# Kernel optimization log

Hardware: AMD Instinct MI355X
Metric: run time of the kernel (lower is better)

## Reference

```python
import jax, jax.numpy as jnp
import numpy as np

N_ATOMS = 50000
N_EDGES = 320000
ATOM_DIM = 32
BOND_DIM = 64


def setup_inputs() -> dict:
    key = jax.random.key(0)
    k1, k2, k3, k4 = jax.random.split(key, 4)
    atom_features = jax.random.normal(k1, (N_ATOMS, ATOM_DIM), dtype=jnp.float32)
    bond_features = jax.random.normal(k2, (N_EDGES, BOND_DIM), dtype=jnp.float32)
    pair_indices = jax.random.randint(k3, (N_EDGES, 2), 0, N_ATOMS, dtype=jnp.int64)
    # Xavier-uniform init for kernel [bond_dim, atom_dim*atom_dim]
    fan_in, fan_out = BOND_DIM, ATOM_DIM * ATOM_DIM
    limit = float(np.sqrt(6.0 / (fan_in + fan_out)))
    kernel = jax.random.uniform(k4, (BOND_DIM, ATOM_DIM * ATOM_DIM), dtype=jnp.float32,
                                minval=-limit, maxval=limit)
    bias = jnp.zeros((ATOM_DIM * ATOM_DIM,), dtype=jnp.float32)
    return {"atom_features": atom_features, "bond_features": bond_features,
            "pair_indices": pair_indices, "kernel": kernel, "bias": bias}


def reference(atom_features, bond_features, pair_indices, kernel, bias):
    d = atom_features.shape[-1]
    # Dense projection: [E, bond_dim] @ [bond_dim, d*d] -> [E, d, d]
    edge_mat = (bond_features @ kernel + bias).reshape(-1, d, d)
    # Gather neighbor features and apply per-edge matrix-vector product
    nbr = atom_features[pair_indices[:, 1]]              # [E, d]
    transformed = jnp.einsum('eij,ej->ei', edge_mat, nbr)  # [E, d]
    # Scatter-add aggregation onto destination atoms
    return jax.ops.segment_sum(transformed, pair_indices[:, 0],
                               num_segments=atom_features.shape[0])
```

## Files before the change

### kernel.cpp

```cpp
#include <hip/hip_runtime.h>
#include <stdint.h>

#define NA 50000
#define NE 320000
#define AD 32
#define BD 64

#define WS_FLAG   0
#define WS_COUNTS 16
#define WS_CURSOR (WS_COUNTS + NA)
#define WS_OFFS   (WS_CURSOR + NA)
#define WS_EIDS   150048
#define WS_NEED_PACKED   ((WS_EIDS + 2 * NE) * 4)
#define WS_NEED_UNPACKED ((WS_EIDS + NE) * 4)

__device__ __forceinline__ void load_pair(const void* p, int e, int mode, int& s, int& d){
  if (mode){ const int* q = (const int*)p; s = q[2*e]; d = q[2*e+1]; }
  else     { const long long* q = (const long long*)p; s = (int)q[2*e]; d = (int)q[2*e+1]; }
}

__global__ void k_detect(const void* pairs, uint32_t* ws){
  const uint32_t* w = (const uint32_t*)pairs;
  uint32_t x = 0;
  for (int i = threadIdx.x; i < 2048; i += 256) x |= w[2*i + 1];
  __shared__ uint32_t sh[256];
  sh[threadIdx.x] = x; __syncthreads();
  for (int s = 128; s > 0; s >>= 1){
    if (threadIdx.x < s) sh[threadIdx.x] |= sh[threadIdx.x + s];
    __syncthreads();
  }
  if (threadIdx.x == 0) ws[WS_FLAG] = (sh[0] != 0u) ? 1u : 0u;
}

__global__ void k_hist(const void* pairs, uint32_t* ws){
  int e = blockIdx.x * 256 + threadIdx.x;
  if (e >= NE) return;
  int mode = (int)ws[WS_FLAG];
  int s, d; load_pair(pairs, e, mode, s, d);
  atomicAdd(&ws[WS_COUNTS + s], 1u);
}

__global__ void k_scan(uint32_t* ws){
  const uint32_t* counts = ws + WS_COUNTS;
  uint32_t* offs = ws + WS_OFFS;
  __shared__ uint32_t wsum[16];
  __shared__ uint32_t carrysh;
  const int tid = threadIdx.x; const int lane = tid & 63; const int wid = tid >> 6;
  if (tid == 0) carrysh = 0u;
  __syncthreads();
  for (int base = 0; base < NA; base += 8192){
    uint32_t v[8]; uint32_t tot = 0u;
    int i0 = base + tid * 8;
    #pragma unroll
    for (int j = 0; j < 8; ++j){ int i = i0 + j; v[j] = (i < NA) ? counts[i] : 0u; tot += v[j]; }
    uint32_t inc = tot;
    #pragma unroll
    for (int m = 1; m < 64; m <<= 1){ uint32_t t = __shfl_up(inc, m); if (lane >= m) inc += t; }
    if (lane == 63) wsum[wid] = inc;
    __syncthreads();
    if (wid == 0){
      uint32_t w = (lane < 16) ? wsum[lane] : 0u;
      #pragma unroll
      for (int m = 1; m < 16; m <<= 1){ uint32_t t = __shfl_up(w, m); if (lane >= m) w += t; }
      if (lane < 16) wsum[lane] = w;
    }
    __syncthreads();
    uint32_t waveoff = (wid == 0) ? 0u : wsum[wid - 1];
    uint32_t run = carrysh + waveoff + (inc - tot);
    #pragma unroll
    for (int j = 0; j < 8; ++j){ int i = i0 + j; if (i < NA) offs[i] = run; run += v[j]; }
    __syncthreads();
    if (tid == 0) carrysh += wsum[15];
    __syncthreads();
  }
  if (tid == 0) offs[NA] = carrysh;
}

template<int PACKED>
__global__ void k_scatter(const void* pairs, uint32_t* ws){
  int e = blockIdx.x * 256 + threadIdx.x;
  if (e >= NE) return;
  int mode = (int)ws[WS_FLAG];
  int s, d; load_pair(pairs, e, mode, s, d);
  uint32_t p = atomicAdd(&ws[WS_CURSOR + s], 1u);
  uint32_t pos = ws[WS_OFFS + s] + p;
  if (PACKED) ((uint2*)(ws + WS_EIDS))[pos] = make_uint2((uint32_t)e, (uint32_t)d);
  else        ws[WS_EIDS + pos] = (uint32_t)e;
}

__launch_bounds__(512, 1)
__global__ void k_main(const float* __restrict__ atoms, const float* __restrict__ bonds,
                       const void* __restrict__ pairs, const float* __restrict__ Kg,
                       const float* __restrict__ bias, float* __restrict__ out,
                       const uint32_t* __restrict__ ws, int packed){
  __shared__ float Ksh[8 * 1024];
  __shared__ float red[8 * 520];

  const int tid  = threadIdx.x;
  const int lane = tid & 63;
  const int wid  = tid >> 6;
  const int kk   = lane & 7;
  const int jq   = lane >> 3;
  const int mode = (int)ws[WS_FLAG];
  const uint32_t* offs = ws + WS_OFFS;

  const int a0 = blockIdx.x * 16 + wid * 2;
  const int a1 = a0 + 1;

  float R0[8][4], R1[8][4], S0[4], S1[4];
  #pragma unroll
  for (int c = 0; c < 8; ++c)
    #pragma unroll
    for (int j = 0; j < 4; ++j){ R0[c][j] = 0.f; R1[c][j] = 0.f; }
  #pragma unroll
  for (int j = 0; j < 4; ++j){ S0[j] = 0.f; S1[j] = 0.f; }

  #pragma unroll
  for (int sel = 0; sel < 2; ++sel){
    const int a = sel ? a1 : a0;
    const uint32_t beg = offs[a];
    const uint32_t n   = offs[a + 1] - beg;
    uint32_t e_nxt = 0, d_nxt = 0;
    if (n){
      if (packed){ uint2 ed = ((const uint2*)(ws + WS_EIDS))[beg]; e_nxt = ed.x; d_nxt = ed.y; }
      else {
        e_nxt = ws[WS_EIDS + beg];
        int s_, d_; load_pair(pairs, (int)e_nxt, mode, s_, d_); d_nxt = (uint32_t)d_;
      }
    }
    for (uint32_t t = 0; t < n; ++t){
      const uint32_t e = e_nxt, d = d_nxt;
      if (t + 1 < n){
        if (packed){ uint2 ed = ((const uint2*)(ws + WS_EIDS))[beg + t + 1]; e_nxt = ed.x; d_nxt = ed.y; }
        else {
          e_nxt = ws[WS_EIDS + beg + t + 1];
          int s_, d_; load_pair(pairs, (int)e_nxt, mode, s_, d_); d_nxt = (uint32_t)d_;
        }
      }
      const float4 av = *(const float4*)&atoms[d * AD + jq * 4];
      const float4 b0 = *(const float4*)&bonds[e * BD + kk * 8];
      const float4 b1 = *(const float4*)&bonds[e * BD + kk * 8 + 4];
      const float b[8] = {b0.x, b0.y, b0.z, b0.w, b1.x, b1.y, b1.z, b1.w};
      if (sel == 0){
        #pragma unroll
        for (int c = 0; c < 8; ++c){
          R0[c][0] += b[c] * av.x; R0[c][1] += b[c] * av.y;
          R0[c][2] += b[c] * av.z; R0[c][3] += b[c] * av.w;
        }
        if (kk == 0){ S0[0] += av.x; S0[1] += av.y; S0[2] += av.z; S0[3] += av.w; }
      } else {
        #pragma unroll
        for (int c = 0; c < 8; ++c){
          R1[c][0] += b[c] * av.x; R1[c][1] += b[c] * av.y;
          R1[c][2] += b[c] * av.z; R1[c][3] += b[c] * av.w;
        }
        if (kk == 0){ S1[0] += av.x; S1[1] += av.y; S1[2] += av.z; S1[3] += av.w; }
      }
    }
  }

  float acc0[32], acc1[32];
  #pragma unroll
  for (int i = 0; i < 32; ++i){ acc0[i] = 0.f; acc1[i] = 0.f; }

  #pragma unroll
  for (int c = 0; c < 8; ++c){
    __syncthreads();
    #pragma unroll
    for (int q = 0; q < 4; ++q){
      const int f4   = tid + q * 512;
      const int word = f4 * 4;
      const int row  = word >> 10;
      const int col  = word & 1023;
      const int sw   = row * 1024 + (col ^ (row << 2));
      *(float4*)&Ksh[sw] = *(const float4*)&Kg[(row * 8 + c) * 1024 + col];
    }
    __syncthreads();
    #pragma unroll
    for (int i = 0; i < 32; ++i){
      const float4 kv = *(const float4*)&Ksh[kk * 1024 + ((i * 32 + jq * 4) ^ (kk << 2))];
      acc0[i] += kv.x * R0[c][0] + kv.y * R0[c][1] + kv.z * R0[c][2] + kv.w * R0[c][3];
      acc1[i] += kv.x * R1[c][0] + kv.y * R1[c][1] + kv.z * R1[c][2] + kv.w * R1[c][3];
    }
  }

  if (kk == 0){
    #pragma unroll
    for (int i = 0; i < 32; ++i){
      const float4 bv = *(const float4*)&bias[i * 32 + jq * 4];
      acc0[i] += bv.x * S0[0] + bv.y * S0[1] + bv.z * S0[2] + bv.w * S0[3];
      acc1[i] += bv.x * S1[0] + bv.y * S1[1] + bv.z * S1[2] + bv.w * S1[3];
    }
  }

  float* myred = &red[wid * 520];
  auto epi = [&](const float (&acc)[32], int a){
    #pragma unroll
    for (int g = 0; g < 4; ++g){
      #pragma unroll
      for (int ii = 0; ii < 8; ++ii) myred[ii * 65 + lane] = acc[g * 8 + ii];
      const int ii = lane & 7, seg = lane >> 3;
      float p = 0.f;
      #pragma unroll
      for (int t2 = 0; t2 < 8; ++t2) p += myred[ii * 65 + seg * 8 + t2];
      p += __shfl_xor(p, 8);
      p += __shfl_xor(p, 16);
      p += __shfl_xor(p, 32);
      if (lane < 8) out[a * 32 + g * 8 + lane] = p;
    }
  };
  epi(acc0, a0);
  epi(acc1, a1);
}

extern "C" void kernel_launch(void* const* d_in, const int* in_sizes, int n_in,
                              void* d_out, int out_size, void* d_ws, size_t ws_size,
                              hipStream_t stream){
  const float* atoms = (const float*)d_in[0];
  const float* bonds = (const float*)d_in[1];
  const void*  pairs = d_in[2];
  const float* Kg    = (const float*)d_in[3];
  const float* bias  = (const float*)d_in[4];
  float* out = (float*)d_out;
  uint32_t* ws = (uint32_t*)d_ws;
  const int packed = (ws_size >= (size_t)WS_NEED_PACKED) ? 1 : 0;

  hipMemsetAsync(ws + WS_COUNTS, 0, sizeof(uint32_t) * 2 * NA, stream);
  k_detect<<<1, 256, 0, stream>>>(pairs, ws);
  k_hist<<<(NE + 255) / 256, 256, 0, stream>>>(pairs, ws);
  k_scan<<<1, 1024, 0, stream>>>(ws);
  if (packed) k_scatter<1><<<(NE + 255) / 256, 256, 0, stream>>>(pairs, ws);
  else        k_scatter<0><<<(NE + 255) / 256, 256, 0, stream>>>(pairs, ws);
  k_main<<<NA / 16, 512, 0, stream>>>(atoms, bonds, pairs, Kg, bias, out, ws, packed);
}
```

Measured before the change: 1.156 ms.

## Halve k_main block size and split output accumulation into two halves

k_main now launches 256-thread blocks covering 8 atoms with launch bounds for 2 blocks per CU, instead of 512-thread blocks covering 16 atoms. The K projection stage is split into two halves of 16 output rows, so each thread keeps 16+16 accumulators instead of 32+32 and the shared K tile shrinks to 16 KB. This lowers register and LDS pressure to allow more resident waves and better latency hiding on the gather loop. In exchange, every block streams the full kernel matrix from global memory twice as often, and the half loop adds extra barriers.

```diff
diff --git a/kernel.cpp b/kernel.cpp
--- a/kernel.cpp
+++ b/kernel.cpp
@@ -11,8 +11,7 @@
 #define WS_CURSOR (WS_COUNTS + NA)
 #define WS_OFFS   (WS_CURSOR + NA)
 #define WS_EIDS   150048
-#define WS_NEED_PACKED   ((WS_EIDS + 2 * NE) * 4)
-#define WS_NEED_UNPACKED ((WS_EIDS + NE) * 4)
+#define WS_NEED_PACKED   ((size_t)(WS_EIDS + 2 * NE) * 4)
 
 __device__ __forceinline__ void load_pair(const void* p, int e, int mode, int& s, int& d){
   if (mode){ const int* q = (const int*)p; s = q[2*e]; d = q[2*e+1]; }
@@ -88,13 +87,26 @@
   else        ws[WS_EIDS + pos] = (uint32_t)e;
 }
 
-__launch_bounds__(512, 1)
+#define RUP(Rm, c, bc) { Rm[c][0] += (bc)*av.x; Rm[c][1] += (bc)*av.y; \
+                         Rm[c][2] += (bc)*av.z; Rm[c][3] += (bc)*av.w; }
+
+#define EPI8(accArr, g, a)                                                      \
+  { _Pragma("unroll")                                                           \
+    for (int ii = 0; ii < 8; ++ii) myred[ii * 65 + lane] = accArr[(g) * 8 + ii];\
+    const int ii2 = lane & 7, seg = lane >> 3;                                  \
+    float p = 0.f;                                                              \
+    _Pragma("unroll")                                                           \
+    for (int t2 = 0; t2 < 8; ++t2) p += myred[ii2 * 65 + seg * 8 + t2];         \
+    p += __shfl_xor(p, 8); p += __shfl_xor(p, 16); p += __shfl_xor(p, 32);      \
+    if (lane < 8) out[(a) * 32 + half * 16 + (g) * 8 + lane] = p; }
+
+__launch_bounds__(256, 2)
 __global__ void k_main(const float* __restrict__ atoms, const float* __restrict__ bonds,
                        const void* __restrict__ pairs, const float* __restrict__ Kg,
                        const float* __restrict__ bias, float* __restrict__ out,
                        const uint32_t* __restrict__ ws, int packed){
-  __shared__ float Ksh[8 * 1024];
-  __shared__ float red[8 * 520];
+  __shared__ float Ksh[8 * 512];
+  __shared__ float red[4 * 520];
 
   const int tid  = threadIdx.x;
   const int lane = tid & 63;
@@ -104,113 +116,102 @@
   const int mode = (int)ws[WS_FLAG];
   const uint32_t* offs = ws + WS_OFFS;
 
-  const int a0 = blockIdx.x * 16 + wid * 2;
+  const int a0 = blockIdx.x * 8 + wid * 2;
   const int a1 = a0 + 1;
 
-  float R0[8][4], R1[8][4], S0[4], S1[4];
+  float R0[8][4], R1[8][4];
   #pragma unroll
   for (int c = 0; c < 8; ++c)
     #pragma unroll
     for (int j = 0; j < 4; ++j){ R0[c][j] = 0.f; R1[c][j] = 0.f; }
-  #pragma unroll
-  for (int j = 0; j < 4; ++j){ S0[j] = 0.f; S1[j] = 0.f; }
-
-  #pragma unroll
-  for (int sel = 0; sel < 2; ++sel){
-    const int a = sel ? a1 : a0;
-    const uint32_t beg = offs[a];
-    const uint32_t n   = offs[a + 1] - beg;
+  float4 S0 = make_float4(0.f,0.f,0.f,0.f);
+  float4 S1 = make_float4(0.f,0.f,0.f,0.f);
+
+  {
+    const uint32_t beg = offs[a0];
+    const uint32_t n   = offs[a0 + 1] - beg;
     uint32_t e_nxt = 0, d_nxt = 0;
     if (n){
       if (packed){ uint2 ed = ((const uint2*)(ws + WS_EIDS))[beg]; e_nxt = ed.x; d_nxt = ed.y; }
-      else {
-        e_nxt = ws[WS_EIDS + beg];
-        int s_, d_; load_pair(pairs, (int)e_nxt, mode, s_, d_); d_nxt = (uint32_t)d_;
-      }
+      else { e_nxt = ws[WS_EIDS + beg]; int s_, d_; load_pair(pairs, (int)e_nxt, mode, s_, d_); d_nxt = (uint32_t)d_; }
     }
     for (uint32_t t = 0; t < n; ++t){
       const uint32_t e = e_nxt, d = d_nxt;
       if (t + 1 < n){
         if (packed){ uint2 ed = ((const uint2*)(ws + WS_EIDS))[beg + t + 1]; e_nxt = ed.x; d_nxt = ed.y; }
-        else {
-          e_nxt = ws[WS_EIDS + beg + t + 1];
-          int s_, d_; load_pair(pairs, (int)e_nxt, mode, s_, d_); d_nxt = (uint32_t)d_;
-        }
-      }
-      const float4 av = *(const float4*)&atoms[d * AD + jq * 4];
-      const float4 b0 = *(const float4*)&bonds[e * BD + kk * 8];
-      const float4 b1 = *(const float4*)&bonds[e * BD + kk * 8 + 4];
-      const float b[8] = {b0.x, b0.y, b0.z, b0.w, b1.x, b1.y, b1.z, b1.w};
-      if (sel == 0){
-        #pragma unroll
-        for (int c = 0; c < 8; ++c){
-          R0[c][0] += b[c] * av.x; R0[c][1] += b[c] * av.y;
-          R0[c][2] += b[c] * av.z; R0[c][3] += b[c] * av.w;
-        }
-        if (kk == 0){ S0[0] += av.x; S0[1] += av.y; S0[2] += av.z; S0[3] += av.w; }
-      } else {
-        #pragma unroll
-        for (int c = 0; c < 8; ++c){
-          R1[c][0] += b[c] * av.x; R1[c][1] += b[c] * av.y;
-          R1[c][2] += b[c] * av.z; R1[c][3] += b[c] * av.w;
-        }
-        if (kk == 0){ S1[0] += av.x; S1[1] += av.y; S1[2] += av.z; S1[3] += av.w; }
-      }
-    }
-  }
-
-  float acc0[32], acc1[32];
-  #pragma unroll
-  for (int i = 0; i < 32; ++i){ acc0[i] = 0.f; acc1[i] = 0.f; }
-
-  #pragma unroll
-  for (int c = 0; c < 8; ++c){
-    __syncthreads();
-    #pragma unroll
-    for (int q = 0; q < 4; ++q){
-      const int f4   = tid + q * 512;
-      const int word = f4 * 4;
-      const int row  = word >> 10;
-      const int col  = word & 1023;
-      const int sw   = row * 1024 + (col ^ (row << 2));
-      *(float4*)&Ksh[sw] = *(const float4*)&Kg[(row * 8 + c) * 1024 + col];
-    }
-    __syncthreads();
-    #pragma unroll
-    for (int i = 0; i < 32; ++i){
-      const float4 kv = *(const float4*)&Ksh[kk * 1024 + ((i * 32 + jq * 4) ^ (kk << 2))];
-      acc0[i] += kv.x * R0[c][0] + kv.y * R0[c][1] + kv.z * R0[c][2] + kv.w * R0[c][3];
-      acc1[i] += kv.x * R1[c][0] + kv.y * R1[c][1] + kv.z * R1[c][2] + kv.w * R1[c][3];
-    }
-  }
-
-  if (kk == 0){
-    #pragma unroll
-    for (int i = 0; i < 32; ++i){
-      const float4 bv = *(const float4*)&bias[i * 32 + jq * 4];
-      acc0[i] += bv.x * S0[0] + bv.y * S0[1] + bv.z * S0[2] + bv.w * S0[3];
-      acc1[i] += bv.x * S1[0] + bv.y * S1[1] + bv.z * S1[2] + bv.w * S1[3];
+        else { e_nxt = ws[WS_EIDS + beg + t + 1]; int s_, d_; load_pair(pairs, (int)e_nxt, mode, s_, d_); d_nxt = (uint32_t)d_; }
+      }
+      const float4 av  = *(const float4*)&atoms[d * AD + jq * 4];
+      const float4 b0v = *(const float4*)&bonds[e * BD + kk * 8];
+      const float4 b1v = *(const float4*)&bonds[e * BD + kk * 8 + 4];
+      RUP(R0, 0, b0v.x) RUP(R0, 1, b0v.y) RUP(R0, 2, b0v.z) RUP(R0, 3, b0v.w)
+      RUP(R0, 4, b1v.x) RUP(R0, 5, b1v.y) RUP(R0, 6, b1v.z) RUP(R0, 7, b1v.w)
+      if (kk == 0){ S0.x += av.x; S0.y += av.y; S0.z += av.z; S0.w += av.w; }
+    }
+  }
+  {
+    const uint32_t beg = offs[a1];
+    const uint32_t n   = offs[a1 + 1] - beg;
+    uint32_t e_nxt = 0, d_nxt = 0;
+    if (n){
+      if (packed){ uint2 ed = ((const uint2*)(ws + WS_EIDS))[beg]; e_nxt = ed.x; d_nxt = ed.y; }
+      else { e_nxt = ws[WS_EIDS + beg]; int s_, d_; load_pair(pairs, (int)e_nxt, mode, s_, d_); d_nxt = (uint32_t)d_; }
+    }
+    for (uint32_t t = 0; t < n; ++t){
+      const uint32_t e = e_nxt, d = d_nxt;
+      if (t + 1 < n){
+        if (packed){ uint2 ed = ((const uint2*)(ws + WS_EIDS))[beg + t + 1]; e_nxt = ed.x; d_nxt = ed.y; }
+        else { e_nxt = ws[WS_EIDS + beg + t + 1]; int s_, d_; load_pair(pairs, (int)e_nxt, mode, s_, d_); d_nxt = (uint32_t)d_; }
+      }
+      const float4 av  = *(const float4*)&atoms[d * AD + jq * 4];
+      const float4 b0v = *(const float4*)&bonds[e * BD + kk * 8];
+      const float4 b1v = *(const float4*)&bonds[e * BD + kk * 8 + 4];
+      RUP(R1, 0, b0v.x) RUP(R1, 1, b0v.y) RUP(R1, 2, b0v.z) RUP(R1, 3, b0v.w)
+      RUP(R1, 4, b1v.x) RUP(R1, 5, b1v.y) RUP(R1, 6, b1v.z) RUP(R1, 7, b1v.w)
+      if (kk == 0){ S1.x += av.x; S1.y += av.y; S1.z += av.z; S1.w += av.w; }
     }
   }
 
   float* myred = &red[wid * 520];
-  auto epi = [&](const float (&acc)[32], int a){
-    #pragma unroll
-    for (int g = 0; g < 4; ++g){
-      #pragma unroll
-      for (int ii = 0; ii < 8; ++ii) myred[ii * 65 + lane] = acc[g * 8 + ii];
-      const int ii = lane & 7, seg = lane >> 3;
-      float p = 0.f;
-      #pragma unroll
-      for (int t2 = 0; t2 < 8; ++t2) p += myred[ii * 65 + seg * 8 + t2];
-      p += __shfl_xor(p, 8);
-      p += __shfl_xor(p, 16);
-      p += __shfl_xor(p, 32);
-      if (lane < 8) out[a * 32 + g * 8 + lane] = p;
-    }
-  };
-  epi(acc0, a0);
-  epi(acc1, a1);
+  for (int half = 0; half < 2; ++half){
+    float aA[16], aB[16];
+    #pragma unroll
+    for (int i = 0; i < 16; ++i){ aA[i] = 0.f; aB[i] = 0.f; }
+
+    #pragma unroll
+    for (int c = 0; c < 8; ++c){
+      __syncthreads();
+      #pragma unroll
+      for (int q = 0; q < 4; ++q){
+        const int idx   = tid + q * 256;
+        const int slot  = idx >> 7;
+        const int col16 = idx & 127;
+        *(float4*)&Ksh[(slot * 128 + (col16 ^ (slot << 3))) * 4] =
+          *(const float4*)&Kg[(slot * 8 + c) * 1024 + half * 512 + col16 * 4];
+      }
+      __syncthreads();
+      #pragma unroll
+      for (int i = 0; i < 16; ++i){
+        const float4 kv = *(const float4*)&Ksh[(kk * 128 + ((i * 8 + jq) ^ (kk << 3))) * 4];
+        aA[i] += kv.x * R0[c][0] + kv.y * R0[c][1] + kv.z * R0[c][2] + kv.w * R0[c][3];
+        aB[i] += kv.x * R1[c][0] + kv.y * R1[c][1] + kv.z * R1[c][2] + kv.w * R1[c][3];
+      }
+    }
+
+    if (kk == 0){
+      #pragma unroll
+      for (int i = 0; i < 16; ++i){
+        const float4 bv = *(const float4*)&bias[(half * 16 + i) * 32 + jq * 4];
+        aA[i] += bv.x * S0.x + bv.y * S0.y + bv.z * S0.z + bv.w * S0.w;
+        aB[i] += bv.x * S1.x + bv.y * S1.y + bv.z * S1.z + bv.w * S1.w;
+      }
+    }
+
+    EPI8(aA, 0, a0)
+    EPI8(aA, 1, a0)
+    EPI8(aB, 0, a1)
+    EPI8(aB, 1, a1)
+  }
 }
 
 extern "C" void kernel_launch(void* const* d_in, const int* in_sizes, int n_in,
@@ -223,7 +224,7 @@
   const float* bias  = (const float*)d_in[4];
   float* out = (float*)d_out;
   uint32_t* ws = (uint32_t*)d_ws;
-  const int packed = (ws_size >= (size_t)WS_NEED_PACKED) ? 1 : 0;
+  const int packed = (ws_size >= WS_NEED_PACKED) ? 1 : 0;
 
   hipMemsetAsync(ws + WS_COUNTS, 0, sizeof(uint32_t) * 2 * NA, stream);
   k_detect<<<1, 256, 0, stream>>>(pairs, ws);
@@ -231,5 +232,5 @@
   k_scan<<<1, 1024, 0, stream>>>(ws);
   if (packed) k_scatter<1><<<(NE + 255) / 256, 256, 0, stream>>>(pairs, ws);
   else        k_scatter<0><<<(NE + 255) / 256, 256, 0, stream>>>(pairs, ws);
-  k_main<<<NA / 16, 512, 0, stream>>>(atoms, bonds, pairs, Kg, bias, out, ws, packed);
-}
+  k_main<<<NA / 8, 256, 0, stream>>>(atoms, bonds, pairs, Kg, bias, out, ws, packed);
+}
```

Result: slower. 3.585 ms (+210.1%).
